# Kernel optimization log

Measured on AMD Instinct MI355X. Metric: run time of the kernel, lower is better.

## Reference

```python
import jax, jax.numpy as jnp
import numpy as np
from jax import lax

DN_CONV = ('NCHW', 'OIHW', 'NCHW')
DN_DECONV = ('NCHW', 'IOHW', 'NCHW')


def _conv(x, w, b, stride, pad):
    y = lax.conv_general_dilated(x, w, (stride, stride), ((pad, pad), (pad, pad)),
                                 dimension_numbers=DN_CONV)
    return y + b[None, :, None, None]


def _deconv(x, w, b):
    # torch ConvTranspose2d(k=4, stride=2, padding=1): equivalent to conv with
    # lhs_dilation=2, padding=k-1-p=2, spatially flipped kernel, weight [Cin,Cout,kH,kW].
    wf = w[:, :, ::-1, ::-1]
    y = lax.conv_general_dilated(x, wf, (1, 1), ((2, 2), (2, 2)),
                                 lhs_dilation=(2, 2), dimension_numbers=DN_DECONV)
    return y + b[None, :, None, None]


def setup_inputs() -> dict:
    key = jax.random.key(0)
    ks = jax.random.split(key, 14)
    s = 0.05
    H, D, K = 128, 64, 512  # hidden, embedding_dim, num_embeddings
    inp = {
        'x': jax.random.normal(ks[0], (32, 3, 256, 256), jnp.float32),
        'enc_w1': jax.random.normal(ks[1], (H, 3, 4, 4), jnp.float32) * s,
        'enc_b1': jnp.zeros((H,), jnp.float32),
        'enc_w2': jax.random.normal(ks[2], (H, H, 4, 4), jnp.float32) * s,
        'enc_b2': jnp.zeros((H,), jnp.float32),
        'enc_w3': jax.random.normal(ks[3], (D, H, 3, 3), jnp.float32) * s,
        'enc_b3': jnp.zeros((D,), jnp.float32),
        'codebook': jax.random.uniform(ks[4], (K, D), jnp.float32, -1.0 / K, 1.0 / K),
        'dec_w1': jax.random.normal(ks[5], (H, D, 3, 3), jnp.float32) * s,
        'dec_b1': jnp.zeros((H,), jnp.float32),
        'dec_w2': jax.random.normal(ks[6], (H, H, 4, 4), jnp.float32) * s,  # [Cin,Cout,4,4]
        'dec_b2': jnp.zeros((H,), jnp.float32),
        'dec_w3': jax.random.normal(ks[7], (H, 3, 4, 4), jnp.float32) * s,  # [Cin,Cout,4,4]
        'dec_b3': jnp.zeros((3,), jnp.float32),
    }
    return inp


def reference(x, enc_w1, enc_b1, enc_w2, enc_b2, enc_w3, enc_b3, codebook,
              dec_w1, dec_b1, dec_w2, dec_b2, dec_w3, dec_b3):
    # encoder
    h = jax.nn.relu(_conv(x, enc_w1, enc_b1, 2, 1))
    h = jax.nn.relu(_conv(h, enc_w2, enc_b2, 2, 1))
    z_e = _conv(h, enc_w3, enc_b3, 1, 1)  # [B, D, 64, 64]

    # vector quantization (faithful to torch .view(-1, D) memory reshape)
    D = codebook.shape[1]
    flat = z_e.reshape(-1, D)  # [N, D]
    d2 = (jnp.sum(flat * flat, axis=1, keepdims=True)
          + jnp.sum(codebook * codebook, axis=1)
          - 2.0 * flat @ codebook.T)  # [N, K]
    idx = jnp.argmin(d2, axis=1)
    z_q = jnp.take(codebook, idx, axis=0).reshape(z_e.shape)

    # decoder
    h = jax.nn.relu(_conv(z_q, dec_w1, dec_b1, 1, 1))
    h = jax.nn.relu(_deconv(h, dec_w2, dec_b2))
    x_recon = _deconv(h, dec_w3, dec_b3)
    return (x_recon, z_e, z_q)
```

## Files before the change

kernel.cpp:

```cpp
#include <hip/hip_runtime.h>
#include <hip/hip_bf16.h>


typedef unsigned short u16;
typedef unsigned int u32;
typedef unsigned long long u64;
typedef __attribute__((ext_vector_type(8))) short short8;
typedef __attribute__((ext_vector_type(4))) float f32x4;

__device__ __forceinline__ float bf2f(u16 u) {
    union { u32 i; float f; } x; x.i = ((u32)u) << 16; return x.f;
}
__device__ __forceinline__ u16 f2bf(float f) {
    __hip_bfloat16 h = __float2bfloat16(f);
    return *reinterpret_cast<u16*>(&h);
}

__global__ void g_k3(const float* __restrict__ w, u16* __restrict__ wg,
                     int CIN, int COUT)
{
    int idx = blockIdx.x * 256 + threadIdx.x;
    if (idx >= 9 * CIN * COUT) return;
    int ci = idx % CIN;
    int co = (idx / CIN) % COUT;
    int s  = idx / (CIN * COUT);
    wg[idx] = f2bf(w[(co * CIN + ci) * 9 + s]);
}

__global__ void g_enc2(const float* __restrict__ w, u16* __restrict__ wg)
{
    int idx = blockIdx.x * 256 + threadIdx.x;
    int ci = idx & 127, co = (idx >> 7) & 127, s = (idx >> 14) & 3, p = idx >> 16;
    int a = p >> 1, b = p & 1, j = s >> 1, i = s & 1;
    int ky = (1 - a) + 2 * j, kx = (1 - b) + 2 * i;
    wg[idx] = f2bf(w[((co << 7 | ci) << 4) + ky * 4 + kx]);
}

__global__ void g_dec2(const float* __restrict__ w, u16* __restrict__ wg)
{
    int idx = blockIdx.x * 256 + threadIdx.x;
    int ci = idx & 127, co = (idx >> 7) & 127, s = (idx >> 14) & 3, p = idx >> 16;
    int py = p >> 1, px = p & 1, j = s >> 1, i = s & 1;
    wg[idx] = f2bf(w[((ci << 7 | co) << 4) + (3 - (py + 2 * j)) * 4 + (3 - (px + 2 * i))]);
}

__global__ void g_dec3m(const float* __restrict__ w, u16* __restrict__ wg)
{
    int idx = blockIdx.x * 256 + threadIdx.x;
    if (idx >= 18432) return;
    int ci  = idx & 127;
    int row = (idx >> 7) & 15;
    int t   = idx >> 11;
    int dy = t / 3 - 1, dx = t % 3 - 1;
    float v = 0.f;
    if (row < 12) {
        int p = row / 3, co = row % 3;
        int py = p >> 1, px = p & 1;
        int a = dy + 1 - py, b2 = dx + 1 - px;
        if (a >= 0 && a <= 1 && b2 >= 0 && b2 <= 1)
            v = w[((ci * 3 + co) * 4 + (3 - (py + 2 * a))) * 4 + (3 - (px + 2 * b2))];
    }
    wg[idx] = f2bf(v);
}

__global__ void g_enc1(const float* __restrict__ w, u16* __restrict__ wg)
{
    int idx = blockIdx.x * 256 + threadIdx.x;
    if (idx >= 8192) return;
    int ci = idx & 3, kx = (idx >> 2) & 3, ky = (idx >> 4) & 3, co = idx >> 6;
    float v = 0.f;
    if (ci < 3) v = w[((co * 3 + ci) * 4 + ky) * 4 + kx];
    wg[idx] = f2bf(v);
}

__global__ void g_cbk(const float* __restrict__ cbk, u16* __restrict__ cb,
                      float* __restrict__ cn)
{
    int idx = blockIdx.x * 256 + threadIdx.x;
    if (idx >= 32768) return;
    cb[idx] = f2bf(cbk[idx]);
    if (idx < 512) {
        float s = 0.f;
        const float* r = cbk + idx * 64;
        for (int i = 0; i < 64; i++) s += r[i] * r[i];
        cn[idx] = s;
    }
}

__global__ __launch_bounds__(256) void xcl_k(
    const float* __restrict__ x, u16* __restrict__ xcl)
{
    const int y = blockIdx.x % 258, n = blockIdx.x / 258;
    const int gy = y - 1;
    for (int xx = threadIdx.x; xx < 258; xx += 256) {
        const int gx = xx - 1;
        u16 pk[4] = {0, 0, 0, 0};
        if (gy >= 0 && gy < 256 && gx >= 0 && gx < 256) {
            const size_t base = ((size_t)n * 3 * 256 + gy) * 256 + gx;
            pk[0] = f2bf(x[base]);
            pk[1] = f2bf(x[base + 65536]);
            pk[2] = f2bf(x[base + 131072]);
        }
        *(u64*)(xcl + ((size_t)(n * 258 + y) * 258 + xx) * 4) = *(const u64*)pk;
    }
}

__global__ __launch_bounds__(256) void enc1m_k(
    const u16* __restrict__ xcl, const u16* __restrict__ wg,
    const float* __restrict__ bias, u16* __restrict__ P)
{
    const int tid = threadIdx.x;
    const int l = tid & 63, w = tid >> 6;
    const int ln = l & 15, kg = l >> 4;
    const int px = w >> 1, half = w & 1;

    const int oy = blockIdx.x & 127;
    const int n  = blockIdx.x >> 7;
    const int p  = (oy & 1) * 2 + px;
    const int yy = oy >> 1;

    short8 af[8][2];
#pragma unroll
    for (int u = 0; u < 8; u++)
#pragma unroll
        for (int s = 0; s < 2; s++)
            af[u][s] = *(const short8*)(wg + ((u * 16 + ln) << 6) + s * 32 + 8 * kg);

    const u16* xn = xcl + (size_t)n * 258 * 258 * 4;
    const int r0 = 2 * oy;

#pragma unroll
    for (int t = 0; t < 2; t++) {
        const int xq = half * 32 + t * 16 + ln;
        const int ox = px + 2 * xq;

        short8 bf[2];
#pragma unroll
        for (int s = 0; s < 2; s++) {
            const int row = r0 + 2 * s + (kg >> 1);
            bf[s] = *(const short8*)(xn + ((size_t)row * 258 + 2 * ox) * 4
                                     + (kg & 1) * 8);
        }

        f32x4 acc[8];
#pragma unroll
        for (int u = 0; u < 8; u++) acc[u] = (f32x4){0.f, 0.f, 0.f, 0.f};
#pragma unroll
        for (int u = 0; u < 8; u++) {
            acc[u] = __builtin_amdgcn_mfma_f32_16x16x32_bf16(af[u][0], bf[0], acc[u], 0, 0, 0);
            acc[u] = __builtin_amdgcn_mfma_f32_16x16x32_bf16(af[u][1], bf[1], acc[u], 0, 0, 0);
        }

#pragma unroll
        for (int u = 0; u < 8; u++) {
            const int cobase = u * 16 + 4 * kg;
            u16 pk[4];
#pragma unroll
            for (int r = 0; r < 4; r++)
                pk[r] = f2bf(fmaxf(acc[u][r] + bias[cobase + r], 0.f));
            *(u64*)(P + ((((size_t)(n * 4 + p) * 64 + yy) * 64 + xq) << 7) + cobase)
                = *(const u64*)pk;
        }
    }
}

template<int J, int I, int NP, int SY, int OUTM>
__global__ __launch_bounds__(256) void conv_mx2(
    const u16* __restrict__ x, const u16* __restrict__ wg,
    const float* __restrict__ bias, void* __restrict__ yv,
    int CIN, int COUT)
{
    constexpr int RS = 2 * SY + 2;
    __shared__ u16 XL[RS * 68 * 40];
    constexpr int NCW = 4 / SY;

    const int tid = threadIdx.x;
    const int l = tid & 63, wv = tid >> 6;
    const int kg = l >> 4, ln = l & 15;
    const int cw = wv % NCW, g = wv / NCW;

    int b = blockIdx.x;
    constexpr int TILES = 64 / (2 * SY);
    const int tile = b % TILES;  b /= TILES;
    const int n = b;
    const int OY0 = tile * (2 * SY);
    const int pc = (OUTM == 2) ? blockIdx.y : 0;

    f32x4 acc[2][8];
#pragma unroll
    for (int u = 0; u < 2; u++)
#pragma unroll
        for (int t = 0; t < 8; t++) acc[u][t] = (f32x4){0.f, 0.f, 0.f, 0.f};

    const u16* xn = x + (size_t)n * NP * CIN * 4096;
    const int co0 = cw * 32 + ln;

    for (int p = 0; p < NP; p++) {
        int dy0, dx0;
        const u16* wgp;
        if (OUTM == 2) {
            dy0 = (pc >> 1) - 1; dx0 = (pc & 1) - 1;
            wgp = wg + (size_t)pc * J * I * COUT * CIN;
        } else if (NP == 4) {
            dy0 = -(p >> 1); dx0 = -(p & 1);
            wgp = wg + (size_t)p * J * I * COUT * CIN;
        } else {
            dy0 = -1; dx0 = -1; wgp = wg;
        }
        const u16* xp = xn + (size_t)p * CIN * 4096;

        for (int ci0 = 0; ci0 < CIN; ci0 += 32) {
            __syncthreads();
            constexpr int TASKS = RS * 68 * 4;
            for (int idx = tid; idx < TASKS; idx += 256) {
                const int q  = idx & 3;
                const int cc = (idx >> 2) % 68;
                const int r  = (idx >> 2) / 68;
                const int gr = OY0 - 1 + r;
                const int gx = cc - 1;
                short8 v = (short8){0, 0, 0, 0, 0, 0, 0, 0};
                if (gr >= 0 && gr < 64 && gx >= 0 && gx < 64)
                    v = *(const short8*)(xp + (size_t)(gr * 64 + gx) * CIN
                                         + ci0 + 8 * q);
                *(short8*)(XL + (r * 68 + cc) * 40 + 8 * q) = v;
            }
            __syncthreads();

#define TAP_ROW(jv)                                                          \
            {                                                                \
                short8 wf0[I], wf1[I];                                       \
                _Pragma("unroll")                                            \
                for (int i = 0; i < I; i++) {                                \
                    const size_t wb = ((size_t)((jv) * I + i) * COUT + co0)  \
                                      * CIN + ci0 + 8 * kg;                  \
                    wf0[i] = *(const short8*)(wgp + wb);                     \
                    wf1[i] = *(const short8*)(wgp + wb + (size_t)16 * CIN);  \
                }                                                            \
                _Pragma("unroll")                                            \
                for (int i = 0; i < I; i++) {                                \
                    _Pragma("unroll")                                        \
                    for (int t = 0; t < 8; t++) {                            \
                        const int rf = (t >> 2) + 2 * g + dy0 + 1 + (jv);    \
                        const int cf = (t & 3) * 16 + ln + dx0 + 1 + i;      \
                        const short8 bf = *(const short8*)(                  \
                            XL + (rf * 68 + cf) * 40 + 8 * kg);              \
                        acc[0][t] = __builtin_amdgcn_mfma_f32_16x16x32_bf16( \
                            wf0[i], bf, acc[0][t], 0, 0, 0);                 \
                        acc[1][t] = __builtin_amdgcn_mfma_f32_16x16x32_bf16( \
                            wf1[i], bf, acc[1][t], 0, 0, 0);                 \
                    }                                                        \
                }                                                            \
            }

            if constexpr (J == 2) {
                TAP_ROW(0); TAP_ROW(1);
            } else {
#pragma unroll 1
                for (int j = 0; j < J; j++) TAP_ROW(j);
            }
#undef TAP_ROW
        }
    }

#pragma unroll
    for (int u = 0; u < 2; u++) {
        const int cob = cw * 32 + u * 16 + 4 * kg;
#pragma unroll
        for (int t = 0; t < 8; t++) {
            const int oy = OY0 + 2 * g + (t >> 2);
            const int ox = (t & 3) * 16 + ln;
            if constexpr (OUTM == 1) {
                float* out = (float*)yv;
#pragma unroll
                for (int rr = 0; rr < 4; rr++)
                    out[(((size_t)n * COUT + cob + rr) * 64 + oy) * 64 + ox]
                        = acc[u][t][rr] + bias[cob + rr];
            } else {
                u16 pk[4];
#pragma unroll
                for (int rr = 0; rr < 4; rr++)
                    pk[rr] = f2bf(fmaxf(acc[u][t][rr] + bias[cob + rr], 0.f));
                if constexpr (OUTM == 0) {
                    *(u64*)((u16*)yv + ((size_t)(n * 64 + oy) * 64 + ox) * COUT
                            + cob) = *(const u64*)pk;
                } else {
                    const int OY = 2 * oy + (pc >> 1), OX = 2 * ox + (pc & 1);
                    *(u64*)((u16*)yv + ((size_t)(n * 128 + OY) * 128 + OX) * 128
                            + cob) = *(const u64*)pk;
                }
            }
        }
    }
}

__global__ __launch_bounds__(256) void dec3m_k(
    const u16* __restrict__ A2, const u16* __restrict__ wg,
    const float* __restrict__ bias, float* __restrict__ out)
{
    const int tid = threadIdx.x;
    const int l = tid & 63, wvi = tid >> 6;
    const int ln = l & 15, kg = l >> 4;

    int b = blockIdx.x;
    const int mxT = b & 7;  b >>= 3;
    const int myT = b & 3;  b >>= 2;
    const int n = b;
    const int X0 = mxT * 16;
    const int MY0 = myT * 32 + wvi * 8;
    const int xx = X0 + ln;

    const short8 z8 = (short8){0, 0, 0, 0, 0, 0, 0, 0};

    f32x4 acc[8];
#pragma unroll
    for (int m = 0; m < 8; m++) acc[m] = (f32x4){0.f, 0.f, 0.f, 0.f};

    int xoff[3]; bool xok[3];
#pragma unroll
    for (int sh = 0; sh < 3; sh++) {
        const int xv = xx + sh - 1;
        xok[sh] = (xv >= 0) & (xv < 128);
        xoff[sh] = (xok[sh] ? xv : 0) << 7;
    }

    for (int ks = 0; ks < 4; ks++) {
        const int cio = ks * 32 + 8 * kg;

        short8 at[9];
#pragma unroll
        for (int t = 0; t < 9; t++)
            at[t] = *(const short8*)(wg + (((size_t)t * 16 + ln) << 7) + cio);

        short8 B[10][3];
#pragma unroll
        for (int r = 0; r < 10; r++) {
            const int yy = MY0 - 1 + r;
            const bool yok = (yy >= 0) & (yy < 128);
            const size_t rowb = ((size_t)(n * 128 + (yok ? yy : 0)) << 7 << 7);
#pragma unroll
            for (int sh = 0; sh < 3; sh++) {
                short8 v = *(const short8*)(A2 + rowb + xoff[sh] + cio);
                B[r][sh] = (yok & xok[sh]) ? v : z8;
            }
            if (r >= 2) {
                const int m = r - 2;
#pragma unroll
                for (int rr = 0; rr < 3; rr++)
#pragma unroll
                    for (int sh = 0; sh < 3; sh++)
                        acc[m] = __builtin_amdgcn_mfma_f32_16x16x32_bf16(
                            at[rr * 3 + sh], B[m + rr][sh], acc[m], 0, 0, 0);
            }
        }
    }

    if (kg < 3) {
#pragma unroll
        for (int m = 0; m < 8; m++) {
            const int my = MY0 + m;
#pragma unroll
            for (int rr = 0; rr < 4; rr++) {
                const int row = 4 * kg + rr;
                const int p = row / 3, co = row % 3;
                const int oy = 2 * my + (p >> 1);
                const int ox = 2 * xx + (p & 1);
                out[(((size_t)(n * 3 + co)) << 16) + oy * 256 + ox]
                    = acc[m][rr] + bias[co];
            }
        }
    }
}

__global__ __launch_bounds__(256) void vqm_k(
    const float* __restrict__ ze, const u16* __restrict__ cb,
    const float* __restrict__ cn, const float* __restrict__ cbk,
    float* __restrict__ zq)
{
    __shared__ float CN[512];
    __shared__ int IDX[64];
    const int tid = threadIdx.x;
    const int l = tid & 63, wvi = tid >> 6;
    const int ln = l & 15, kg = l >> 4;

    for (int i = tid; i < 512; i += 256) CN[i] = cn[i];
    __syncthreads();

    const int V0 = blockIdx.x * 64 + wvi * 16;

    short8 az[2];
#pragma unroll
    for (int ks = 0; ks < 2; ks++) {
        const float* zp = ze + (size_t)(V0 + ln) * 64 + ks * 32 + 8 * kg;
        short8 t;
#pragma unroll
        for (int j = 0; j < 8; j++) t[j] = (short)f2bf(zp[j]);
        az[ks] = t;
    }

    float bval[4] = {3.4e38f, 3.4e38f, 3.4e38f, 3.4e38f};
    int bidx[4] = {0, 0, 0, 0};
    for (int nt = 0; nt < 32; nt++) {
        const int code = nt * 16 + ln;
        const short8 b0 = *(const short8*)(cb + (size_t)code * 64 + 8 * kg);
        const short8 b1 = *(const short8*)(cb + (size_t)code * 64 + 32 + 8 * kg);
        f32x4 d = (f32x4){0.f, 0.f, 0.f, 0.f};
        d = __builtin_amdgcn_mfma_f32_16x16x32_bf16(az[0], b0, d, 0, 0, 0);
        d = __builtin_amdgcn_mfma_f32_16x16x32_bf16(az[1], b1, d, 0, 0, 0);
        const float cnv = CN[code];
#pragma unroll
        for (int r = 0; r < 4; r++) {
            const float dist = cnv - 2.f * d[r];
            if (dist < bval[r]) { bval[r] = dist; bidx[r] = code; }
        }
    }
#pragma unroll
    for (int off = 1; off < 16; off <<= 1) {
#pragma unroll
        for (int r = 0; r < 4; r++) {
            const float ov = __shfl_xor(bval[r], off);
            const int oi = __shfl_xor(bidx[r], off);
            if (ov < bval[r] || (ov == bval[r] && oi < bidx[r])) {
                bval[r] = ov; bidx[r] = oi;
            }
        }
    }
    if (ln == 0) {
#pragma unroll
        for (int r = 0; r < 4; r++) IDX[wvi * 16 + 4 * kg + r] = bidx[r];
    }
    __syncthreads();

    const int vs = tid >> 2, ch = tid & 3;
    const int bi = IDX[vs];
    const float4* sp = (const float4*)(cbk + (size_t)bi * 64 + ch * 16);
    float4* dp = (float4*)(zq + ((size_t)blockIdx.x * 64 + vs) * 64 + ch * 16);
#pragma unroll
    for (int q = 0; q < 4; q++) dp[q] = sp[q];
}

__global__ __launch_bounds__(256) void zqt_k(
    const float* __restrict__ zq, u16* __restrict__ out)
{
    __shared__ float t[64][65];
    const int tid = threadIdx.x;
    const int n = blockIdx.x >> 6, y = blockIdx.x & 63;
    for (int idx = tid; idx < 4096; idx += 256) {
        int xx = idx & 63, ci = idx >> 6;
        t[ci][xx] = zq[(((size_t)n * 64 + ci) * 64 + y) * 64 + xx];
    }
    __syncthreads();
    for (int idx = tid; idx < 4096; idx += 256) {
        int ci = idx & 63, xx = idx >> 6;
        out[(((size_t)n * 64 + y) * 64 + xx) * 64 + ci] = f2bf(t[ci][xx]);
    }
}

extern "C" void kernel_launch(void* const* d_in, const int* in_sizes, int n_in,
                              void* d_out, int out_size, void* d_ws, size_t ws_size,
                              hipStream_t stream)
{
    (void)in_sizes; (void)n_in; (void)out_size; (void)ws_size;

    const float* x   = (const float*)d_in[0];
    const float* ew1 = (const float*)d_in[1];
    const float* eb1 = (const float*)d_in[2];
    const float* ew2 = (const float*)d_in[3];
    const float* eb2 = (const float*)d_in[4];
    const float* ew3 = (const float*)d_in[5];
    const float* eb3 = (const float*)d_in[6];
    const float* cbk = (const float*)d_in[7];
    const float* dw1 = (const float*)d_in[8];
    const float* db1 = (const float*)d_in[9];
    const float* dw2 = (const float*)d_in[10];
    const float* db2 = (const float*)d_in[11];
    const float* dw3 = (const float*)d_in[12];
    const float* db3 = (const float*)d_in[13];

    u16* P    = (u16*)d_ws;
    u16* ZQCL = P;
    u16* A2   = P;
    u16* B = (u16*)((char*)d_ws + 134217728);
    u16* XCL = B;
    u16* Wg2 = (u16*)((char*)d_ws + 167772160);
    u16* Wg3 = Wg2 + 262144;
    u16* Wg4 = Wg3 + 73728;
    u16* Wg5 = Wg4 + 73728;
    u16* Wg6 = Wg5 + 262144;
    u16* CB  = Wg6 + 32768;
    u16* Wg1 = CB + 32768;
    float* CNg = (float*)(Wg1 + 8192);

    float* xr = (float*)d_out;
    float* ze = xr + (size_t)32 * 3 * 256 * 256;
    float* zq = ze + (size_t)32 * 64 * 64 * 64;

    g_enc1<<<32, 256, 0, stream>>>(ew1, Wg1);
    g_enc2<<<1024, 256, 0, stream>>>(ew2, Wg2);
    g_k3<<<288, 256, 0, stream>>>(ew3, Wg3, 128, 64);
    g_k3<<<288, 256, 0, stream>>>(dw1, Wg4, 64, 128);
    g_dec2<<<1024, 256, 0, stream>>>(dw2, Wg5);
    g_dec3m<<<72, 256, 0, stream>>>(dw3, Wg6);
    g_cbk<<<128, 256, 0, stream>>>(cbk, CB, CNg);

    xcl_k<<<32 * 258, 256, 0, stream>>>(x, XCL);
    enc1m_k<<<32 * 128, 256, 0, stream>>>(XCL, Wg1, eb1, P);
    conv_mx2<2, 2, 4, 1, 0><<<32 * 32, 256, 0, stream>>>(P, Wg2, eb2, B, 128, 128);
    conv_mx2<3, 3, 1, 2, 1><<<16 * 32, 256, 0, stream>>>(B, Wg3, eb3, ze, 128, 64);
    vqm_k<<<2048, 256, 0, stream>>>(ze, CB, CNg, cbk, zq);
    zqt_k<<<2048, 256, 0, stream>>>(zq, ZQCL);
    conv_mx2<3, 3, 1, 1, 0><<<32 * 32, 256, 0, stream>>>(ZQCL, Wg4, db1, B, 64, 128);
    conv_mx2<2, 2, 1, 1, 2><<<dim3(32 * 32, 4), 256, 0, stream>>>(B, Wg5, db2, A2, 128, 128);
    dec3m_k<<<1024, 256, 0, stream>>>(A2, Wg6, db3, xr);
}
```

Before: 590.2 us.

## Double-buffer input tile via register prefetch and widen conv blocks to 512 threads

Replaces conv_mx2 with conv_mx3, which uses 512-thread blocks covering twice as many output rows per block. This halves the grid and improves reuse of the halo rows across waves. The next channel chunk's input is prefetched into registers while the current chunk runs on MFMA, and gather offsets are precomputed once. Channel count becomes a template constant and the 3-row tap loop is fully unrolled. The cost is more register pressure and fewer blocks per launch.

```diff
diff --git a/kernel.cpp b/kernel.cpp
--- a/kernel.cpp
+++ b/kernel.cpp
@@ -164,15 +164,19 @@
     }
 }
 
-template<int J, int I, int NP, int SY, int OUTM>
-__global__ __launch_bounds__(256) void conv_mx2(
+template<int J, int I, int NP, int NCW, int CI, int OUTM>
+__global__ __launch_bounds__(512) void conv_mx3(
     const u16* __restrict__ x, const u16* __restrict__ wg,
     const float* __restrict__ bias, void* __restrict__ yv,
-    int CIN, int COUT)
-{
-    constexpr int RS = 2 * SY + 2;
+    int COUT)
+{
+    constexpr int G = 8 / NCW;
+    constexpr int RS = 2 * G + 2;
+    constexpr int TASKS = RS * 68 * 4;
+    constexpr int SLOTS = (TASKS + 511) / 512;
+    constexpr int CHP = CI / 32;
+    constexpr int NCHUNK = NP * CHP;
     __shared__ u16 XL[RS * 68 * 40];
-    constexpr int NCW = 4 / SY;
 
     const int tid = threadIdx.x;
     const int l = tid & 63, wv = tid >> 6;
@@ -180,86 +184,105 @@
     const int cw = wv % NCW, g = wv / NCW;
 
     int b = blockIdx.x;
-    constexpr int TILES = 64 / (2 * SY);
+    constexpr int TILES = 64 / (2 * G);
     const int tile = b % TILES;  b /= TILES;
     const int n = b;
-    const int OY0 = tile * (2 * SY);
+    const int OY0 = tile * (2 * G);
     const int pc = (OUTM == 2) ? blockIdx.y : 0;
 
+    bool valid[SLOTS], okm[SLOTS];
+    int goff[SLOTS], loff[SLOTS];
+#pragma unroll
+    for (int s = 0; s < SLOTS; s++) {
+        const int idx = s * 512 + tid;
+        valid[s] = idx < TASKS;
+        const int q = idx & 3, cc = (idx >> 2) % 68, r = (idx >> 2) / 68;
+        const int gr = OY0 - 1 + r, gx = cc - 1;
+        okm[s] = valid[s] && gr >= 0 && gr < 64 && gx >= 0 && gx < 64;
+        goff[s] = okm[s] ? ((gr * 64 + gx) * CI + 8 * q) : 0;
+        loff[s] = (r * 68 + cc) * 40 + 8 * q;
+    }
+
     f32x4 acc[2][8];
 #pragma unroll
     for (int u = 0; u < 2; u++)
 #pragma unroll
         for (int t = 0; t < 8; t++) acc[u][t] = (f32x4){0.f, 0.f, 0.f, 0.f};
 
-    const u16* xn = x + (size_t)n * NP * CIN * 4096;
+    const u16* xn = x + (size_t)n * NP * CI * 4096;
     const int co0 = cw * 32 + ln;
-
-    for (int p = 0; p < NP; p++) {
+    const short8 z8 = (short8){0, 0, 0, 0, 0, 0, 0, 0};
+
+    short8 pf[SLOTS];
+    {
+        const u16* xp = xn;
+#pragma unroll
+        for (int s = 0; s < SLOTS; s++)
+            pf[s] = okm[s] ? *(const short8*)(xp + goff[s]) : z8;
+    }
+
+    for (int c = 0; c < NCHUNK; c++) {
+        __syncthreads();
+#pragma unroll
+        for (int s = 0; s < SLOTS; s++)
+            if (valid[s]) *(short8*)(XL + loff[s]) = pf[s];
+        __syncthreads();
+
+        if (c + 1 < NCHUNK) {
+            const int cn_ = c + 1;
+            const u16* xp = xn + (size_t)(cn_ / CHP) * CI * 4096
+                            + (cn_ % CHP) * 32;
+#pragma unroll
+            for (int s = 0; s < SLOTS; s++)
+                pf[s] = okm[s] ? *(const short8*)(xp + goff[s]) : z8;
+        }
+
+        const int p = c / CHP;
+        const int ci0 = (c % CHP) * 32;
         int dy0, dx0;
         const u16* wgp;
         if (OUTM == 2) {
             dy0 = (pc >> 1) - 1; dx0 = (pc & 1) - 1;
-            wgp = wg + (size_t)pc * J * I * COUT * CIN;
+            wgp = wg + (size_t)pc * J * I * COUT * CI;
         } else if (NP == 4) {
             dy0 = -(p >> 1); dx0 = -(p & 1);
-            wgp = wg + (size_t)p * J * I * COUT * CIN;
+            wgp = wg + (size_t)p * J * I * COUT * CI;
         } else {
             dy0 = -1; dx0 = -1; wgp = wg;
         }
-        const u16* xp = xn + (size_t)p * CIN * 4096;
-
-        for (int ci0 = 0; ci0 < CIN; ci0 += 32) {
-            __syncthreads();
-            constexpr int TASKS = RS * 68 * 4;
-            for (int idx = tid; idx < TASKS; idx += 256) {
-                const int q  = idx & 3;
-                const int cc = (idx >> 2) % 68;
-                const int r  = (idx >> 2) / 68;
-                const int gr = OY0 - 1 + r;
-                const int gx = cc - 1;
-                short8 v = (short8){0, 0, 0, 0, 0, 0, 0, 0};
-                if (gr >= 0 && gr < 64 && gx >= 0 && gx < 64)
-                    v = *(const short8*)(xp + (size_t)(gr * 64 + gx) * CIN
-                                         + ci0 + 8 * q);
-                *(short8*)(XL + (r * 68 + cc) * 40 + 8 * q) = v;
-            }
-            __syncthreads();
 
 #define TAP_ROW(jv)                                                          \
-            {                                                                \
-                short8 wf0[I], wf1[I];                                       \
+        {                                                                    \
+            short8 wf0[I], wf1[I];                                           \
+            _Pragma("unroll")                                                \
+            for (int i = 0; i < I; i++) {                                    \
+                const size_t wb = ((size_t)((jv) * I + i) * COUT + co0)      \
+                                  * CI + ci0 + 8 * kg;                       \
+                wf0[i] = *(const short8*)(wgp + wb);                         \
+                wf1[i] = *(const short8*)(wgp + wb + (size_t)16 * CI);       \
+            }                                                                \
+            _Pragma("unroll")                                                \
+            for (int i = 0; i < I; i++) {                                    \
                 _Pragma("unroll")                                            \
-                for (int i = 0; i < I; i++) {                                \
-                    const size_t wb = ((size_t)((jv) * I + i) * COUT + co0)  \
-                                      * CIN + ci0 + 8 * kg;                  \
-                    wf0[i] = *(const short8*)(wgp + wb);                     \
-                    wf1[i] = *(const short8*)(wgp + wb + (size_t)16 * CIN);  \
+                for (int t = 0; t < 8; t++) {                                \
+                    const int rf = (t >> 2) + 2 * g + dy0 + 1 + (jv);        \
+                    const int cf = (t & 3) * 16 + ln + dx0 + 1 + i;          \
+                    const short8 bf = *(const short8*)(                      \
+                        XL + (rf * 68 + cf) * 40 + 8 * kg);                  \
+                    acc[0][t] = __builtin_amdgcn_mfma_f32_16x16x32_bf16(     \
+                        wf0[i], bf, acc[0][t], 0, 0, 0);                     \
+                    acc[1][t] = __builtin_amdgcn_mfma_f32_16x16x32_bf16(     \
+                        wf1[i], bf, acc[1][t], 0, 0, 0);                     \
                 }                                                            \
-                _Pragma("unroll")                                            \
-                for (int i = 0; i < I; i++) {                                \
-                    _Pragma("unroll")                                        \
-                    for (int t = 0; t < 8; t++) {                            \
-                        const int rf = (t >> 2) + 2 * g + dy0 + 1 + (jv);    \
-                        const int cf = (t & 3) * 16 + ln + dx0 + 1 + i;      \
-                        const short8 bf = *(const short8*)(                  \
-                            XL + (rf * 68 + cf) * 40 + 8 * kg);              \
-                        acc[0][t] = __builtin_amdgcn_mfma_f32_16x16x32_bf16( \
-                            wf0[i], bf, acc[0][t], 0, 0, 0);                 \
-                        acc[1][t] = __builtin_amdgcn_mfma_f32_16x16x32_bf16( \
-                            wf1[i], bf, acc[1][t], 0, 0, 0);                 \
-                    }                                                        \
-                }                                                            \
-            }
-
-            if constexpr (J == 2) {
-                TAP_ROW(0); TAP_ROW(1);
-            } else {
-#pragma unroll 1
-                for (int j = 0; j < J; j++) TAP_ROW(j);
-            }
+            }                                                                \
+        }
+
+        if constexpr (J == 2) {
+            TAP_ROW(0); TAP_ROW(1);
+        } else {
+            TAP_ROW(0); TAP_ROW(1); TAP_ROW(2);
+        }
 #undef TAP_ROW
-        }
     }
 
 #pragma unroll
@@ -504,11 +527,11 @@
 
     xcl_k<<<32 * 258, 256, 0, stream>>>(x, XCL);
     enc1m_k<<<32 * 128, 256, 0, stream>>>(XCL, Wg1, eb1, P);
-    conv_mx2<2, 2, 4, 1, 0><<<32 * 32, 256, 0, stream>>>(P, Wg2, eb2, B, 128, 128);
-    conv_mx2<3, 3, 1, 2, 1><<<16 * 32, 256, 0, stream>>>(B, Wg3, eb3, ze, 128, 64);
+    conv_mx3<2, 2, 4, 4, 128, 0><<<32 * 16, 512, 0, stream>>>(P, Wg2, eb2, B, 128);
+    conv_mx3<3, 3, 1, 2, 128, 1><<<32 * 8, 512, 0, stream>>>(B, Wg3, eb3, ze, 64);
     vqm_k<<<2048, 256, 0, stream>>>(ze, CB, CNg, cbk, zq);
     zqt_k<<<2048, 256, 0, stream>>>(zq, ZQCL);
-    conv_mx2<3, 3, 1, 1, 0><<<32 * 32, 256, 0, stream>>>(ZQCL, Wg4, db1, B, 64, 128);
-    conv_mx2<2, 2, 1, 1, 2><<<dim3(32 * 32, 4), 256, 0, stream>>>(B, Wg5, db2, A2, 128, 128);
+    conv_mx3<3, 3, 1, 4, 64, 0><<<32 * 16, 512, 0, stream>>>(ZQCL, Wg4, db1, B, 128);
+    conv_mx3<2, 2, 1, 4, 128, 2><<<dim3(32 * 16, 4), 512, 0, stream>>>(B, Wg5, db2, A2, 128);
     dec3m_k<<<1024, 256, 0, stream>>>(A2, Wg6, db3, xr);
 }
```

Measured after the change: 572.1 us. -3.1%, faster.
